# Performance work log

Measured on AMD Instinct MI355X. Metric: run time of the kernel, lower is better.

## Reference

```python
import jax, jax.numpy as jnp
import numpy as np

N_GROUP = 4
TOPK_GROUP = 2
TOP_K = 6
ROUTED_SCALE = 2.0

T, H, E, I = 1024, 1024, 16, 704
SHARED_I = 2 * H  # n_shared_experts * hidden_size


def setup_inputs() -> dict:
    key = jax.random.key(0)
    ks = jax.random.split(key, 10)
    s = 0.02
    return {
        "h": jax.random.normal(ks[0], (T, H), jnp.float32),
        "gate_w": jax.random.normal(ks[1], (E, H), jnp.float32) * s,
        "bias": jax.random.normal(ks[2], (E,), jnp.float32) * 0.1,
        "wg": jax.random.normal(ks[3], (E, H, I), jnp.float32) * s,
        "wu": jax.random.normal(ks[4], (E, H, I), jnp.float32) * s,
        "wd": jax.random.normal(ks[5], (E, I, H), jnp.float32) * s,
        "swg": jax.random.normal(ks[6], (H, SHARED_I), jnp.float32) * s,
        "swu": jax.random.normal(ks[7], (H, SHARED_I), jnp.float32) * s,
        "swd": jax.random.normal(ks[8], (SHARED_I, H), jnp.float32) * s,
    }


def _moe_forward(h, gate_w, bias, wg, wu, wd, swg, swu, swd):
    Tn, Hd = h.shape
    En = gate_w.shape[0]
    per_group = En // N_GROUP

    # shared expert (SwiGLU MLP)
    shared = (jax.nn.silu(h @ swg) * (h @ swu)) @ swd  # [T, H]

    # gate: noaux_tc biased grouped top-k routing (DeepSeek-V3 style)
    logits = h @ gate_w.T                      # [T, E]
    scores = jax.nn.sigmoid(logits)            # [T, E]
    scores_for_choice = scores + bias[None, :]
    grp = scores_for_choice.reshape(Tn, N_GROUP, per_group)
    group_scores = jnp.sum(jax.lax.top_k(grp, 2)[0], axis=-1)   # [T, G] top-2 sum
    _, top_groups = jax.lax.top_k(group_scores, TOPK_GROUP)     # [T, TG]
    gmask = jnp.zeros((Tn, N_GROUP), bool).at[
        jnp.arange(Tn)[:, None], top_groups].set(True)
    emask = jnp.repeat(gmask, per_group, axis=1)                # [T, E]
    masked = jnp.where(emask, scores_for_choice, -jnp.inf)
    _, topk_ids = jax.lax.top_k(masked, TOP_K)                  # [T, K]
    topk_w = jnp.take_along_axis(scores, topk_ids, axis=1)      # weights from unbiased scores
    topk_w = topk_w / jnp.sum(topk_w, axis=-1, keepdims=True)   # norm_topk_prob=True

    # sparse combine weights [T, E]
    cw = jnp.zeros((Tn, En), h.dtype).at[
        jnp.arange(Tn)[:, None], topk_ids].add(topk_w)

    # per-expert SwiGLU MLPs (dense over experts, sparse combine)
    g = jnp.einsum('th,ehi->tei', h, wg)
    u = jnp.einsum('th,ehi->tei', h, wu)
    y = jnp.einsum('tei,eih->teh', jax.nn.silu(g) * u, wd)
    routed = jnp.einsum('te,teh->th', cw, y)

    return routed * ROUTED_SCALE + shared


def reference(h, gate_w, bias, wg, wu, wd, swg, swu, swd):
    return _moe_forward(h, gate_w, bias, wg, wu, wd, swg, swu, swd)
```

## Files before the change

kernel.cpp:

```cpp
#include <hip/hip_runtime.h>
#include <hip/hip_bf16.h>
#include <math.h>

#define TT 1024
#define HH 1024
#define NEXP 16
#define NI 704
#define SI 2048
#define UPMAX 506
#define WDTILES 1408
#define DNSHARED 64
#define DNMAX (DNSHARED + 504)

typedef unsigned short us;
typedef __attribute__((ext_vector_type(8))) __bf16 bf16x8;
typedef __attribute__((ext_vector_type(4))) float f32x4;
typedef __attribute__((ext_vector_type(4))) unsigned short us4;

__device__ __forceinline__ us f2bf(float f) {
  unsigned u = __builtin_bit_cast(unsigned, f);
  u += 0x7fffu + ((u >> 16) & 1u);
  return (us)(u >> 16);
}

__device__ __forceinline__ int ldsOff(int row, int kg) {
  return (row * 4 + (kg ^ ((row >> 1) & 3))) * 16;
}

__device__ __forceinline__ void gl16(const void* g, void* l) {
  __builtin_amdgcn_global_load_lds((const __attribute__((address_space(1))) void*)g,
                                   (__attribute__((address_space(3))) void*)l, 16, 0, 0);
}

__device__ __forceinline__ int chunkMap(int b, int n) {
  int q = n >> 3, r = n & 7;
  int c = b & 7, i = b >> 3;
  int base = (c < r) ? c * (q + 1) : r * (q + 1) + (c - r) * q;
  return base + i;
}

__device__ __forceinline__ void tconv_tile(const float* __restrict__ inz,
                                           us* __restrict__ outz,
                                           int C, int ldo, int r0, int c0,
                                           float (*tile)[65]) {
  int t = threadIdx.x;
  int rr = t >> 4, cc = (t & 15) * 4;
  #pragma unroll
  for (int i = 0; i < 4; ++i) {
    f32x4 v = *reinterpret_cast<const f32x4*>(inz + (size_t)(r0 + rr + i * 16) * C + c0 + cc);
    tile[rr + i*16][cc + 0] = v[0];
    tile[rr + i*16][cc + 1] = v[1];
    tile[rr + i*16][cc + 2] = v[2];
    tile[rr + i*16][cc + 3] = v[3];
  }
  __syncthreads();
  int c = t >> 2, rq = t & 3;
  us o0[8], o1[8];
  #pragma unroll
  for (int j = 0; j < 8; ++j) {
    o0[j] = f2bf(tile[rq * 16 + j][c]);
    o1[j] = f2bf(tile[rq * 16 + 8 + j][c]);
  }
  us* op = outz + (size_t)(c0 + c) * ldo + r0 + rq * 16;
  *reinterpret_cast<us4*>(op)      = *reinterpret_cast<us4*>(&o0[0]);
  *reinterpret_cast<us4*>(op + 4)  = *reinterpret_cast<us4*>(&o0[4]);
  *reinterpret_cast<us4*>(op + 8)  = *reinterpret_cast<us4*>(&o1[0]);
  *reinterpret_cast<us4*>(op + 12) = *reinterpret_cast<us4*>(&o1[4]);
}

__device__ __forceinline__ void tconv512(const float* __restrict__ inz,
                                         us* __restrict__ outz,
                                         int i0, int h0, float (*tile)[129]) {
  int t = threadIdx.x;
  int ir = t >> 3, cg = (t & 7) * 4;
  #pragma unroll
  for (int p = 0; p < 4; ++p) {
    f32x4 v = *reinterpret_cast<const f32x4*>(inz + (size_t)(i0 + ir) * HH + h0 + cg + p * 32);
    tile[ir][cg + p*32 + 0] = v[0];
    tile[ir][cg + p*32 + 1] = v[1];
    tile[ir][cg + p*32 + 2] = v[2];
    tile[ir][cg + p*32 + 3] = v[3];
  }
  __syncthreads();
  int c = t >> 2, rq = t & 3;
  us o[16];
  #pragma unroll
  for (int j = 0; j < 16; ++j) o[j] = f2bf(tile[rq * 16 + j][c]);
  us* op = outz + (size_t)(h0 + c) * NI + i0 + rq * 16;
  *reinterpret_cast<us4*>(op)      = *reinterpret_cast<us4*>(&o[0]);
  *reinterpret_cast<us4*>(op + 4)  = *reinterpret_cast<us4*>(&o[4]);
  *reinterpret_cast<us4*>(op + 8)  = *reinterpret_cast<us4*>(&o[8]);
  *reinterpret_cast<us4*>(op + 12) = *reinterpret_cast<us4*>(&o[12]);
}

__global__ __launch_bounds__(256) void k_prep(
    const float* __restrict__ h, const float* __restrict__ gw,
    const float* __restrict__ bias, float* __restrict__ cw,
    us* __restrict__ hb, unsigned* __restrict__ selpk,
    const float* __restrict__ wg, const float* __restrict__ wu,
    const float* __restrict__ swg, const float* __restrict__ swu,
    us* __restrict__ wgb, us* __restrict__ wub,
    us* __restrict__ swgb, us* __restrict__ swub) {
  __shared__ float tile[64][65];
  __shared__ float lgS[NEXP];
  int b = blockIdx.x;
  int tid = threadIdx.x;
  if (b < 1024) {
    int t = b;
    const float* hr = h + (size_t)t * HH;
    {
      f32x4 v = *reinterpret_cast<const f32x4*>(hr + tid * 4);
      us4 p;
      p[0] = f2bf(v[0]); p[1] = f2bf(v[1]); p[2] = f2bf(v[2]); p[3] = f2bf(v[3]);
      *reinterpret_cast<us4*>(hb + (size_t)t * HH + tid * 4) = p;
    }
    int e = tid >> 4, sub = tid & 15;
    const f32x4* hr4 = reinterpret_cast<const f32x4*>(hr);
    const f32x4* gr4 = reinterpret_cast<const f32x4*>(gw + (size_t)e * HH);
    float acc = 0.f;
    for (int i = sub; i < 256; i += 16) {
      f32x4 a = hr4[i], g = gr4[i];
      acc += a[0]*g[0] + a[1]*g[1] + a[2]*g[2] + a[3]*g[3];
    }
    acc += __shfl_down(acc, 8, 16);
    acc += __shfl_down(acc, 4, 16);
    acc += __shfl_down(acc, 2, 16);
    acc += __shfl_down(acc, 1, 16);
    if (sub == 0) lgS[e] = acc;
    __syncthreads();
    if (tid == 0) {
      float sc[NEXP], s4[NEXP];
      for (int i = 0; i < NEXP; ++i) {
        sc[i] = 1.f / (1.f + expf(-lgS[i]));
        s4[i] = sc[i] + bias[i];
      }
      float gs[4];
      for (int g = 0; g < 4; ++g) {
        float a = s4[4*g], bb = s4[4*g+1], c = s4[4*g+2], d = s4[4*g+3];
        float mx01 = fmaxf(a, bb), mn01 = fminf(a, bb);
        float mx23 = fmaxf(c, d), mn23 = fminf(c, d);
        float top = fmaxf(mx01, mx23);
        float sec = (mx01 >= mx23) ? fmaxf(mn01, mx23) : fmaxf(mn23, mx01);
        gs[g] = top + sec;
      }
      int g1 = 0;
      for (int g = 1; g < 4; ++g) if (gs[g] > gs[g1]) g1 = g;
      int g2 = -1;
      for (int g = 0; g < 4; ++g) { if (g == g1) continue; if (g2 < 0 || gs[g] > gs[g2]) g2 = g; }
      int sel[6];
      bool used[NEXP];
      for (int i = 0; i < NEXP; ++i) used[i] = false;
      float wsum = 0.f;
      for (int it = 0; it < 6; ++it) {
        int best = -1; float bv = 0.f;
        for (int i = 0; i < NEXP; ++i) {
          int grp = i >> 2;
          if ((grp != g1 && grp != g2) || used[i]) continue;
          if (best < 0 || s4[i] > bv) { best = i; bv = s4[i]; }
        }
        used[best] = true;
        sel[it] = best;
        wsum += sc[best];
      }
      float inv = 2.0f / wsum;
      unsigned pk = 0;
      for (int it = 0; it < 6; ++it) {
        pk |= (unsigned)sel[it] << (it * 4);
        cw[(size_t)t * NEXP + sel[it]] = sc[sel[it]] * inv;
      }
      selpk[t] = pk;
    }
    return;
  }
  b -= 1024;
  if (b < 2816) {
    int z = b / 176, r = b % 176;
    tconv_tile(wg + (size_t)z * HH * NI, wgb + (size_t)z * NI * HH,
               NI, HH, (r / 11) * 64, (r % 11) * 64, tile);
    return;
  }
  b -= 2816;
  if (b < 2816) {
    int z = b / 176, r = b % 176;
    tconv_tile(wu + (size_t)z * HH * NI, wub + (size_t)z * NI * HH,
               NI, HH, (r / 11) * 64, (r % 11) * 64, tile);
    return;
  }
  b -= 2816;
  if (b < 512) {
    tconv_tile(swg, swgb, SI, HH, (b >> 5) * 64, (b & 31) * 64, tile);
    return;
  }
  b -= 512;
  {
    tconv_tile(swu, swub, SI, HH, (b >> 5) * 64, (b & 31) * 64, tile);
  }
}

__global__ void k_scan(const unsigned* __restrict__ selpk,
                       int* __restrict__ cnt, int* __restrict__ list,
                       int* __restrict__ wlUp, int* __restrict__ wlDn,
                       int* __restrict__ totals) {
  int t = threadIdx.x;
  int w = t >> 6, l = t & 63;
  unsigned pk = selpk[t];
  unsigned short flags = 0;
  #pragma unroll
  for (int j = 0; j < 6; ++j) flags |= (unsigned short)(1u << ((pk >> (j * 4)) & 15));
  __shared__ int wc[16][16];
  __shared__ int pre[16][16];
  __shared__ int tiles_s[16], upo[16], dno[16], totR[2];
  #pragma unroll
  for (int e = 0; e < 16; ++e) {
    unsigned long long bal = __ballot((flags >> e) & 1);
    if (l == 0) wc[w][e] = __popcll(bal);
  }
  __syncthreads();
  if (t < 16) {
    int s = 0;
    for (int ww = 0; ww < 16; ++ww) { pre[ww][t] = s; s += wc[ww][t]; }
    cnt[t] = s;
    tiles_s[t] = (s + 127) >> 7;
  }
  __syncthreads();
  if (t < 16) {
    int uo = 0, dn = 0;
    for (int e2 = 0; e2 < t; ++e2) { uo += 6 * tiles_s[e2]; dn += 8 * tiles_s[e2]; }
    upo[t] = uo; dno[t] = dn;
    if (t == 15) { totR[0] = uo + 6 * tiles_s[15]; totR[1] = dn + 8 * tiles_s[15]; }
  }
  __syncthreads();
  {
    int te = tiles_s[w];
    for (int i = l; i < 6 * te; i += 64) {
      int nt = i / te, mt = i - nt * te;
      wlUp[upo[w] + i] = ((w * 6 + nt) << 3) | mt;
    }
    for (int i = l; i < 8 * te; i += 64) {
      int nt = i / te, mt = i - nt * te;
      wlDn[dno[w] + i] = ((w * 8 + nt) << 3) | mt;
    }
  }
  if (w == 0) {
    for (int j = l; j < 128; j += 64)
      wlUp[totR[0] + j] = ((96 + (j >> 3)) << 3) | (j & 7);
  }
  if (t == 0) { totals[0] = totR[0] + 128; totals[1] = totR[1]; }
  unsigned long long lmask = (l == 0) ? 0ull : ((~0ull) >> (64 - l));
  #pragma unroll
  for (int e = 0; e < 16; ++e) {
    bool f = (flags >> e) & 1;
    unsigned long long bal = __ballot(f);
    if (f) {
      int rank = __popcll(bal & lmask);
      int j = 0;
      #pragma unroll
      for (int jj = 0; jj < 6; ++jj) j += (((pk >> (jj * 4)) & 15) == (unsigned)e) ? jj : 0;
      list[(e << 10) + pre[w][e] + rank] = (t << 3) | j;
    }
  }
}

__global__ void k_tconvS(const float* __restrict__ swd, us* __restrict__ swdT) {
  __shared__ float tile[64][65];
  int b = blockIdx.x;
  tconv_tile(swd, swdT, HH, SI, (b >> 4) * 64, (b & 15) * 64, tile);
}

__global__ __launch_bounds__(512) void k_upT(
    const us* __restrict__ hb,
    const us* __restrict__ wgb, const us* __restrict__ wub,
    const us* __restrict__ swgb, const us* __restrict__ swub,
    const float* __restrict__ cw, const int* __restrict__ list,
    const int* __restrict__ cnt, const int* __restrict__ wlUp,
    const int* __restrict__ totals,
    us* __restrict__ cact_r, us* __restrict__ cact_s,
    const float* __restrict__ wd, us* __restrict__ wdbT) {
  __shared__ __align__(16) char ldsb[49152];
  int tid = threadIdx.x;
  if ((int)blockIdx.x >= UPMAX) {
    int b = blockIdx.x - UPMAX;
    int z = b / 88, r = b % 88;
    tconv512(wd + (size_t)z * NI * HH, wdbT + (size_t)z * HH * NI,
             (r >> 3) * 64, (r & 7) * 128,
             reinterpret_cast<float(*)[129]>(ldsb));
    return;
  }
  int tot = totals[0];
  if ((int)blockIdx.x >= tot) return;
  int item = wlUp[chunkMap(blockIdx.x, tot)];
  int group = item >> 3, mt = item & 7;
  int t0 = mt * 128;
  bool routed = group < 96;
  int e = 0, n0, cntE = TT;
  const us *bgBase, *buBase;
  if (routed) {
    e = group / 6;
    n0 = (group - e * 6) * 128;
    cntE = cnt[e];
    bgBase = wgb + (size_t)e * NI * HH;
    buBase = wub + (size_t)e * NI * HH;
  } else {
    n0 = (group - 96) * 128;
    bgBase = swgb;
    buBase = swub;
  }
  int w = tid >> 6, l = tid & 63;
  int wm = w >> 2, wn = w & 3;
  int lr = l & 15, lg2 = l >> 4;

  int rowA = tid >> 2;
  int kg = (tid & 3) ^ ((rowA >> 1) & 3);
  int tok = t0 + rowA;
  if (routed) tok = (tok < cntE) ? (list[(e << 10) + tok] >> 3) : 0;
  int bRow = n0 + rowA;
  if (routed && bRow >= NI) bRow = NI - 1;
  const us* aS = hb + (size_t)tok * HH + kg * 8;
  const us* gS = bgBase + (size_t)bRow * HH + kg * 8;
  const us* uS = buBase + (size_t)bRow * HH + kg * 8;

  f32x4 accG[4][2] = {};
  f32x4 accU[4][2] = {};

  int wslot = w * 1024;
  auto stage = [&](char* buf) {
    char* b = buf + wslot;
    gl16(aS, b);
    gl16(gS, b + 8192);
    gl16(uS, b + 16384);
    aS += 32; gS += 32; uS += 32;
  };

  char* bufR = ldsb;
  char* bufW = ldsb + 24576;
  stage(bufR);
  __syncthreads();
  #pragma unroll 2
  for (int ki = 0; ki < 32; ++ki) {
    if (ki < 31) stage(bufW);
    bf16x8 af[4], bg[2], bu[2];
    #pragma unroll
    for (int rf = 0; rf < 4; ++rf)
      af[rf] = *reinterpret_cast<const bf16x8*>(bufR + ldsOff(wm * 64 + rf * 16 + lr, lg2));
    #pragma unroll
    for (int cf = 0; cf < 2; ++cf) {
      int n = wn * 32 + cf * 16 + lr;
      bg[cf] = *reinterpret_cast<const bf16x8*>(bufR + 8192  + ldsOff(n, lg2));
      bu[cf] = *reinterpret_cast<const bf16x8*>(bufR + 16384 + ldsOff(n, lg2));
    }
    #pragma unroll
    for (int rf = 0; rf < 4; ++rf)
      #pragma unroll
      for (int cf = 0; cf < 2; ++cf) {
        accG[rf][cf] = __builtin_amdgcn_mfma_f32_16x16x32_bf16(af[rf], bg[cf], accG[rf][cf], 0, 0, 0);
        accU[rf][cf] = __builtin_amdgcn_mfma_f32_16x16x32_bf16(af[rf], bu[cf], accU[rf][cf], 0, 0, 0);
      }
    __syncthreads();
    char* tp = bufR; bufR = bufW; bufW = tp;
  }
  #pragma unroll
  for (int rf = 0; rf < 4; ++rf)
    #pragma unroll
    for (int cf = 0; cf < 2; ++cf)
      #pragma unroll
      for (int r = 0; r < 4; ++r) {
        int row = wm * 64 + rf * 16 + lg2 * 4 + r;
        int col = wn * 32 + cf * 16 + lr;
        float g = accG[rf][cf][r], u = accU[rf][cf][r];
        float act = g / (1.f + __expf(-g)) * u;
        if (routed) {
          int slot = t0 + row;
          if (slot < cntE && n0 + col < NI) {
            int packed = list[(e << 10) + slot];
            float scl = cw[(size_t)(packed >> 3) * NEXP + e];
            cact_r[((size_t)(e << 10) + slot) * NI + n0 + col] = f2bf(act * scl);
          }
        } else {
          cact_s[(size_t)(t0 + row) * SI + n0 + col] = f2bf(act);
        }
      }
}

__global__ __launch_bounds__(256) void k_down(
    const us* __restrict__ cact_r, const us* __restrict__ cact_s,
    const us* __restrict__ wdbT, const us* __restrict__ swdT,
    const int* __restrict__ list, const int* __restrict__ cnt,
    const int* __restrict__ wlDn, const int* __restrict__ totals,
    us* __restrict__ part, float* __restrict__ out) {
  __shared__ __align__(16) char ldsb[32768];
  int tid = threadIdx.x;
  int b = blockIdx.x;
  bool routed;
  int e = 0, nt, mt, kiter, Ksrc, cntE = TT;
  const us *Ab, *Bb;
  if (b < DNSHARED) {
    routed = false;
    nt = b & 7;
    mt = b >> 3;
    kiter = 64;
    Ksrc = SI;
    Ab = cact_s;
    Bb = swdT;
  } else {
    routed = true;
    int rb = b - DNSHARED;
    int tot = totals[1];
    if (rb >= tot) return;
    int item = wlDn[chunkMap(rb, tot)];
    int group = item >> 3;
    mt = item & 7;
    e = group >> 3; nt = group & 7;
    cntE = cnt[e];
    kiter = NI / 32;
    Ksrc = NI;
    Ab = cact_r + (size_t)e * 1024 * NI;
    Bb = wdbT + (size_t)e * 1024 * NI;
  }
  int t0 = mt * 128;
  int n0 = nt * 128;
  int w = tid >> 6, l = tid & 63;
  int wm = w >> 1, wn = w & 1;
  int lr = l & 15, lg2 = l >> 4;

  int rowA = tid >> 2;
  int kg = (tid & 3) ^ ((rowA >> 1) & 3);
  const us* aS0 = Ab + (size_t)(t0 + rowA) * Ksrc + kg * 8;
  const us* aS1 = Ab + (size_t)(t0 + 64 + rowA) * Ksrc + kg * 8;
  const us* bS0 = Bb + (size_t)(n0 + rowA) * Ksrc + kg * 8;
  const us* bS1 = Bb + (size_t)(n0 + 64 + rowA) * Ksrc + kg * 8;

  f32x4 acc[4][4] = {};

  int wslot = w * 1024;
  auto stage = [&](char* buf) {
    char* bp = buf + wslot;
    gl16(aS0, bp);
    gl16(aS1, bp + 4096);
    gl16(bS0, bp + 8192);
    gl16(bS1, bp + 12288);
    aS0 += 32; aS1 += 32; bS0 += 32; bS1 += 32;
  };

  char* bufR = ldsb;
  char* bufW = ldsb + 16384;
  stage(bufR);
  __syncthreads();
  for (int ki = 0; ki < kiter; ++ki) {
    if (ki + 1 < kiter) stage(bufW);
    bf16x8 af[4], bb[4];
    #pragma unroll
    for (int rf = 0; rf < 4; ++rf)
      af[rf] = *reinterpret_cast<const bf16x8*>(bufR + ldsOff(wm * 64 + rf * 16 + lr, lg2));
    #pragma unroll
    for (int cf = 0; cf < 4; ++cf)
      bb[cf] = *reinterpret_cast<const bf16x8*>(bufR + 8192 + ldsOff(wn * 64 + cf * 16 + lr, lg2));
    #pragma unroll
    for (int rf = 0; rf < 4; ++rf)
      #pragma unroll
      for (int cf = 0; cf < 4; ++cf)
        acc[rf][cf] = __builtin_amdgcn_mfma_f32_16x16x32_bf16(af[rf], bb[cf], acc[rf][cf], 0, 0, 0);
    __syncthreads();
    char* tp = bufR; bufR = bufW; bufW = tp;
  }
  #pragma unroll
  for (int rf = 0; rf < 4; ++rf)
    #pragma unroll
    for (int cf = 0; cf < 4; ++cf)
      #pragma unroll
      for (int r = 0; r < 4; ++r) {
        int row = wm * 64 + rf * 16 + lg2 * 4 + r;
        int col = wn * 64 + cf * 16 + lr;
        if (routed) {
          int slot = t0 + row;
          if (slot < cntE) {
            int packed = list[(e << 10) + slot];
            int t = packed >> 3, j = packed & 7;
            part[((size_t)t * 6 + j) * 1024 + n0 + col] = f2bf(acc[rf][cf][r]);
          }
        } else {
          out[(size_t)(t0 + row) * HH + n0 + col] = acc[rf][cf][r];
        }
      }
}

__global__ void k_reduce(const us* __restrict__ part, float* __restrict__ out) {
  int i = (blockIdx.x * blockDim.x + threadIdx.x) * 4;
  int t = i >> 10, hh = i & 1023;
  f32x4 s = *reinterpret_cast<const f32x4*>(out + i);
  #pragma unroll
  for (int j = 0; j < 6; ++j) {
    us4 p = *reinterpret_cast<const us4*>(part + ((size_t)t * 6 + j) * 1024 + hh);
    #pragma unroll
    for (int k = 0; k < 4; ++k)
      s[k] += __builtin_bit_cast(float, (unsigned)p[k] << 16);
  }
  *reinterpret_cast<f32x4*>(out + i) = s;
}

#define HB_OFF    0ULL
#define CW_OFF    2097152ULL
#define CNT_OFF   2162688ULL
#define SELPK_OFF 2166784ULL
#define LIST_OFF  2170880ULL
#define WLUP_OFF  2236416ULL
#define WLDN_OFF  2244608ULL
#define TOT_OFF   2252800ULL
#define CACTR_OFF 2260992ULL
#define CACTS_OFF 25329664ULL
#define WGB_OFF   29523968ULL
#define WUB_OFF   52592640ULL
#define SWGB_OFF  75661312ULL
#define SWUB_OFF  79855616ULL
#define WDBT_OFF  84049920ULL
#define SWDT_OFF  SWGB_OFF
#define PART_OFF  WGB_OFF

extern "C" void kernel_launch(void* const* d_in, const int* in_sizes, int n_in,
                              void* d_out, int out_size, void* d_ws, size_t ws_size,
                              hipStream_t stream) {
  const float* h    = (const float*)d_in[0];
  const float* gw   = (const float*)d_in[1];
  const float* bias = (const float*)d_in[2];
  const float* wg   = (const float*)d_in[3];
  const float* wu   = (const float*)d_in[4];
  const float* wd   = (const float*)d_in[5];
  const float* swg  = (const float*)d_in[6];
  const float* swu  = (const float*)d_in[7];
  const float* swd  = (const float*)d_in[8];
  float* out = (float*)d_out;

  char* ws = (char*)d_ws;
  us*       hb     = (us*)(ws + HB_OFF);
  float*    cw     = (float*)(ws + CW_OFF);
  int*      cnt    = (int*)(ws + CNT_OFF);
  unsigned* selpk  = (unsigned*)(ws + SELPK_OFF);
  int*      list   = (int*)(ws + LIST_OFF);
  int*      wlUp   = (int*)(ws + WLUP_OFF);
  int*      wlDn   = (int*)(ws + WLDN_OFF);
  int*      totals = (int*)(ws + TOT_OFF);
  us*       cact_r = (us*)(ws + CACTR_OFF);
  us*       cact_s = (us*)(ws + CACTS_OFF);
  us*       wgb    = (us*)(ws + WGB_OFF);
  us*       wub    = (us*)(ws + WUB_OFF);
  us*       swgb   = (us*)(ws + SWGB_OFF);
  us*       swub   = (us*)(ws + SWUB_OFF);
  us*       wdbT   = (us*)(ws + WDBT_OFF);
  us*       swdT   = (us*)(ws + SWDT_OFF);
  us*       part   = (us*)(ws + PART_OFF);

  k_prep<<<7680, 256, 0, stream>>>(h, gw, bias, cw, hb, selpk,
                                   wg, wu, swg, swu, wgb, wub, swgb, swub);
  k_scan<<<1, 1024, 0, stream>>>(selpk, cnt, list, wlUp, wlDn, totals);

  k_upT<<<UPMAX + WDTILES, 512, 0, stream>>>(hb, wgb, wub, swgb, swub, cw, list,
                                             cnt, wlUp, totals, cact_r, cact_s,
                                             wd, wdbT);

  k_tconvS<<<512, 256, 0, stream>>>(swd, swdT);

  k_down<<<DNMAX, 256, 0, stream>>>(cact_r, cact_s, wdbT, swdT, list, cnt,
                                    wlDn, totals, part, out);
  k_reduce<<<1024, 256, 0, stream>>>(part, out);
}
```

Before: 138.9 us.

## Enlarge up-projection tiles to 256 tokens and rework LDS staging

The routed and shared up-projection GEMM tiles grow from 128 to 256 token rows per block. The scan kernel now builds the up-projection work list with 256-row tiles while the down-projection keeps 128-row tiles, and UPMAX shrinks to match. This halves the number of B-weight tile loads per token and raises MFMA work per LDS load. In exchange each block uses 64KB of LDS and twice as many accumulator registers, which can lower occupancy and load balance across fewer blocks. The LDS swizzle is simplified and the syncthreads are replaced by an explicit vmcnt wait plus s_barrier.

```diff
diff --git a/kernel.cpp b/kernel.cpp
--- a/kernel.cpp
+++ b/kernel.cpp
@@ -7,7 +7,7 @@
 #define NEXP 16
 #define NI 704
 #define SI 2048
-#define UPMAX 506
+#define UPMAX 448
 #define WDTILES 1408
 #define DNSHARED 64
 #define DNMAX (DNSHARED + 504)
@@ -209,7 +209,7 @@
   for (int j = 0; j < 6; ++j) flags |= (unsigned short)(1u << ((pk >> (j * 4)) & 15));
   __shared__ int wc[16][16];
   __shared__ int pre[16][16];
-  __shared__ int tiles_s[16], upo[16], dno[16], totR[2];
+  __shared__ int t128[16], t256[16], upo[16], dno[16], totR[2];
   #pragma unroll
   for (int e = 0; e < 16; ++e) {
     unsigned long long bal = __ballot((flags >> e) & 1);
@@ -220,32 +220,34 @@
     int s = 0;
     for (int ww = 0; ww < 16; ++ww) { pre[ww][t] = s; s += wc[ww][t]; }
     cnt[t] = s;
-    tiles_s[t] = (s + 127) >> 7;
+    t128[t] = (s + 127) >> 7;
+    t256[t] = (s + 255) >> 8;
   }
   __syncthreads();
   if (t < 16) {
     int uo = 0, dn = 0;
-    for (int e2 = 0; e2 < t; ++e2) { uo += 6 * tiles_s[e2]; dn += 8 * tiles_s[e2]; }
+    for (int e2 = 0; e2 < t; ++e2) { uo += 6 * t256[e2]; dn += 8 * t128[e2]; }
     upo[t] = uo; dno[t] = dn;
-    if (t == 15) { totR[0] = uo + 6 * tiles_s[15]; totR[1] = dn + 8 * tiles_s[15]; }
+    if (t == 15) { totR[0] = uo + 6 * t256[15]; totR[1] = dn + 8 * t128[15]; }
   }
   __syncthreads();
   {
-    int te = tiles_s[w];
-    for (int i = l; i < 6 * te; i += 64) {
-      int nt = i / te, mt = i - nt * te;
+    int teU = t256[w];
+    for (int i = l; i < 6 * teU; i += 64) {
+      int nt = i / teU, mt = i - nt * teU;
       wlUp[upo[w] + i] = ((w * 6 + nt) << 3) | mt;
     }
-    for (int i = l; i < 8 * te; i += 64) {
-      int nt = i / te, mt = i - nt * te;
+    int teD = t128[w];
+    for (int i = l; i < 8 * teD; i += 64) {
+      int nt = i / teD, mt = i - nt * teD;
       wlDn[dno[w] + i] = ((w * 8 + nt) << 3) | mt;
     }
   }
   if (w == 0) {
-    for (int j = l; j < 128; j += 64)
-      wlUp[totR[0] + j] = ((96 + (j >> 3)) << 3) | (j & 7);
-  }
-  if (t == 0) { totals[0] = totR[0] + 128; totals[1] = totR[1]; }
+    for (int j = l; j < 64; j += 64)
+      wlUp[totR[0] + j] = ((96 + (j >> 2)) << 3) | (j & 3);
+  }
+  if (t == 0) { totals[0] = totR[0] + 64; totals[1] = totR[1]; }
   unsigned long long lmask = (l == 0) ? 0ull : ((~0ull) >> (64 - l));
   #pragma unroll
   for (int e = 0; e < 16; ++e) {
@@ -276,7 +278,7 @@
     const int* __restrict__ totals,
     us* __restrict__ cact_r, us* __restrict__ cact_s,
     const float* __restrict__ wd, us* __restrict__ wdbT) {
-  __shared__ __align__(16) char ldsb[49152];
+  __shared__ __align__(16) char ldsb[65536];
   int tid = threadIdx.x;
   if ((int)blockIdx.x >= UPMAX) {
     int b = blockIdx.x - UPMAX;
@@ -290,7 +292,7 @@
   if ((int)blockIdx.x >= tot) return;
   int item = wlUp[chunkMap(blockIdx.x, tot)];
   int group = item >> 3, mt = item & 7;
-  int t0 = mt * 128;
+  int t0 = mt * 256;
   bool routed = group < 96;
   int e = 0, n0, cntE = TT;
   const us *bgBase, *buBase;
@@ -309,62 +311,76 @@
   int wm = w >> 2, wn = w & 3;
   int lr = l & 15, lg2 = l >> 4;
 
-  int rowA = tid >> 2;
-  int kg = (tid & 3) ^ ((rowA >> 1) & 3);
-  int tok = t0 + rowA;
-  if (routed) tok = (tok < cntE) ? (list[(e << 10) + tok] >> 3) : 0;
-  int bRow = n0 + rowA;
-  if (routed && bRow >= NI) bRow = NI - 1;
-  const us* aS = hb + (size_t)tok * HH + kg * 8;
-  const us* gS = bgBase + (size_t)bRow * HH + kg * 8;
-  const us* uS = buBase + (size_t)bRow * HH + kg * 8;
-
-  f32x4 accG[4][2] = {};
-  f32x4 accU[4][2] = {};
-
+  const us *s0, *s1, *s2, *s3;
+  {
+    int row0 = tid >> 2;
+    int kgA = (tid & 3) ^ (row0 & 3);
+    int sl0 = t0 + row0;
+    int tok0 = routed ? ((sl0 < cntE) ? (list[(e << 10) + sl0] >> 3) : 0) : sl0;
+    s0 = hb + (size_t)tok0 * HH + kgA * 8;
+    int sl1 = sl0 + 128;
+    int tok1 = routed ? ((sl1 < cntE) ? (list[(e << 10) + sl1] >> 3) : 0) : sl1;
+    s1 = hb + (size_t)tok1 * HH + kgA * 8;
+    int brow = n0 + row0;
+    if (routed && brow >= NI) brow = NI - 1;
+    s2 = bgBase + (size_t)brow * HH + kgA * 8;
+    s3 = buBase + (size_t)brow * HH + kgA * 8;
+  }
   int wslot = w * 1024;
-  auto stage = [&](char* buf) {
-    char* b = buf + wslot;
-    gl16(aS, b);
-    gl16(gS, b + 8192);
-    gl16(uS, b + 16384);
-    aS += 32; gS += 32; uS += 32;
+  auto stageAll = [&](char* buf) {
+    gl16(s0, buf + wslot);
+    gl16(s1, buf + 8192 + wslot);
+    gl16(s2, buf + 16384 + wslot);
+    gl16(s3, buf + 24576 + wslot);
+    s0 += 32; s1 += 32; s2 += 32; s3 += 32;
   };
 
-  char* bufR = ldsb;
-  char* bufW = ldsb + 24576;
-  stage(bufR);
-  __syncthreads();
-  #pragma unroll 2
-  for (int ki = 0; ki < 32; ++ki) {
-    if (ki < 31) stage(bufW);
-    bf16x8 af[4], bg[2], bu[2];
-    #pragma unroll
-    for (int rf = 0; rf < 4; ++rf)
-      af[rf] = *reinterpret_cast<const bf16x8*>(bufR + ldsOff(wm * 64 + rf * 16 + lr, lg2));
+  f32x4 accG[8][2] = {};
+  f32x4 accU[8][2] = {};
+
+  int sw16 = (lg2 ^ (lr & 3)) * 16;
+  int aoff = lr * 64 + sw16;
+  int boff = lr * 64 + sw16;
+
+  char* cur = ldsb;
+  char* nxt = ldsb + 32768;
+  stageAll(cur);
+  asm volatile("s_waitcnt vmcnt(0)" ::: "memory");
+  __builtin_amdgcn_s_barrier();
+  asm volatile("" ::: "memory");
+
+  for (int t = 0; t < 32; ++t) {
+    if (t < 31) stageAll(nxt);
+    bf16x8 af[8], bg[2], bu[2];
+    #pragma unroll
+    for (int rf = 0; rf < 8; ++rf)
+      af[rf] = *reinterpret_cast<const bf16x8*>(cur + (wm * 128 + rf * 16) * 64 + aoff);
     #pragma unroll
     for (int cf = 0; cf < 2; ++cf) {
-      int n = wn * 32 + cf * 16 + lr;
-      bg[cf] = *reinterpret_cast<const bf16x8*>(bufR + 8192  + ldsOff(n, lg2));
-      bu[cf] = *reinterpret_cast<const bf16x8*>(bufR + 16384 + ldsOff(n, lg2));
-    }
-    #pragma unroll
-    for (int rf = 0; rf < 4; ++rf)
+      int rb = (wn * 32 + cf * 16) * 64 + boff;
+      bg[cf] = *reinterpret_cast<const bf16x8*>(cur + 16384 + rb);
+      bu[cf] = *reinterpret_cast<const bf16x8*>(cur + 24576 + rb);
+    }
+    #pragma unroll
+    for (int rf = 0; rf < 8; ++rf)
       #pragma unroll
       for (int cf = 0; cf < 2; ++cf) {
         accG[rf][cf] = __builtin_amdgcn_mfma_f32_16x16x32_bf16(af[rf], bg[cf], accG[rf][cf], 0, 0, 0);
         accU[rf][cf] = __builtin_amdgcn_mfma_f32_16x16x32_bf16(af[rf], bu[cf], accU[rf][cf], 0, 0, 0);
       }
-    __syncthreads();
-    char* tp = bufR; bufR = bufW; bufW = tp;
-  }
-  #pragma unroll
-  for (int rf = 0; rf < 4; ++rf)
+    asm volatile("s_waitcnt vmcnt(0)" ::: "memory");
+    __builtin_amdgcn_s_barrier();
+    asm volatile("" ::: "memory");
+    char* tp = cur; cur = nxt; nxt = tp;
+  }
+
+  #pragma unroll
+  for (int rf = 0; rf < 8; ++rf)
     #pragma unroll
     for (int cf = 0; cf < 2; ++cf)
       #pragma unroll
       for (int r = 0; r < 4; ++r) {
-        int row = wm * 64 + rf * 16 + lg2 * 4 + r;
+        int row = wm * 128 + rf * 16 + lg2 * 4 + r;
         int col = wn * 32 + cf * 16 + lr;
         float g = accG[rf][cf][r], u = accU[rf][cf][r];
         float act = g / (1.f + __expf(-g)) * u;
```

New measurement: 157.3 us. +13.2%, slower.

## Triple-buffer up-projection K loop with explicit vmcnt waits and MFMA priority

Applied to the files above, without the earlier changes.

Switches the up-projection GEMM main loop from double to triple buffering of the async global-to-LDS tiles, so two stages are in flight. Fine-grained s_waitcnt vmcnt counts and raw s_barrier replace __syncthreads, which previously drained all memory ops. It also raises wave priority around the MFMA block. The LDS footprint grows from 48KB to 72KB per block, which may reduce occupancy, and the wait counts assume exactly three loads per stage.

```diff
diff --git a/kernel.cpp b/kernel.cpp
--- a/kernel.cpp
+++ b/kernel.cpp
@@ -276,7 +276,7 @@
     const int* __restrict__ totals,
     us* __restrict__ cact_r, us* __restrict__ cact_s,
     const float* __restrict__ wd, us* __restrict__ wdbT) {
-  __shared__ __align__(16) char ldsb[49152];
+  __shared__ __align__(16) char ldsb[73728];
   int tid = threadIdx.x;
   if ((int)blockIdx.x >= UPMAX) {
     int b = blockIdx.x - UPMAX;
@@ -331,23 +331,33 @@
     aS += 32; gS += 32; uS += 32;
   };
 
-  char* bufR = ldsb;
-  char* bufW = ldsb + 24576;
-  stage(bufR);
-  __syncthreads();
-  #pragma unroll 2
+  char* bA = ldsb;
+  char* bB = ldsb + 24576;
+  char* bC = ldsb + 49152;
+  stage(bA);
+  stage(bB);
   for (int ki = 0; ki < 32; ++ki) {
-    if (ki < 31) stage(bufW);
+    if (ki < 30) {
+      stage(bC);
+      asm volatile("s_waitcnt vmcnt(6)" ::: "memory");
+    } else if (ki == 30) {
+      asm volatile("s_waitcnt vmcnt(3)" ::: "memory");
+    } else {
+      asm volatile("s_waitcnt vmcnt(0)" ::: "memory");
+    }
+    __builtin_amdgcn_s_barrier();
+    asm volatile("" ::: "memory");
     bf16x8 af[4], bg[2], bu[2];
     #pragma unroll
     for (int rf = 0; rf < 4; ++rf)
-      af[rf] = *reinterpret_cast<const bf16x8*>(bufR + ldsOff(wm * 64 + rf * 16 + lr, lg2));
+      af[rf] = *reinterpret_cast<const bf16x8*>(bA + ldsOff(wm * 64 + rf * 16 + lr, lg2));
     #pragma unroll
     for (int cf = 0; cf < 2; ++cf) {
       int n = wn * 32 + cf * 16 + lr;
-      bg[cf] = *reinterpret_cast<const bf16x8*>(bufR + 8192  + ldsOff(n, lg2));
-      bu[cf] = *reinterpret_cast<const bf16x8*>(bufR + 16384 + ldsOff(n, lg2));
-    }
+      bg[cf] = *reinterpret_cast<const bf16x8*>(bA + 8192  + ldsOff(n, lg2));
+      bu[cf] = *reinterpret_cast<const bf16x8*>(bA + 16384 + ldsOff(n, lg2));
+    }
+    __builtin_amdgcn_s_setprio(1);
     #pragma unroll
     for (int rf = 0; rf < 4; ++rf)
       #pragma unroll
@@ -355,8 +365,10 @@
         accG[rf][cf] = __builtin_amdgcn_mfma_f32_16x16x32_bf16(af[rf], bg[cf], accG[rf][cf], 0, 0, 0);
         accU[rf][cf] = __builtin_amdgcn_mfma_f32_16x16x32_bf16(af[rf], bu[cf], accU[rf][cf], 0, 0, 0);
       }
-    __syncthreads();
-    char* tp = bufR; bufR = bufW; bufW = tp;
+    __builtin_amdgcn_s_setprio(0);
+    __builtin_amdgcn_s_barrier();
+    asm volatile("" ::: "memory");
+    char* tp = bA; bA = bB; bB = bC; bC = tp;
   }
   #pragma unroll
   for (int rf = 0; rf < 4; ++rf)
```

After: 136.8 us. Within noise of the previous version (-1.5%).
